# Kernel optimization log

Hardware: AMD Instinct MI355X
Metric: run time of the kernel (lower is better)

## Reference

```python
import jax, jax.numpy as jnp
import numpy as np

PI = np.pi


def ramp_filter(x):
    """skimage-style ramp filter along the detector axis (axis=2).
    x: [B, C, D, A] sinogram."""
    D = x.shape[2]
    P = max(64, int(2 ** np.ceil(np.log2(2 * D))))  # padded FFT size
    xp = jnp.pad(x, ((0, 0), (0, 0), (0, P - D), (0, 0)))
    # real-space ramp kernel (Kak & Slaney), then FFT -> frequency filter
    n = np.concatenate([np.arange(1, P // 2 + 1, 2), np.arange(P // 2 - 1, 0, -2)])
    f = np.zeros(P, dtype=np.float64)
    f[0] = 0.25
    f[1::2] = -1.0 / (PI * n) ** 2
    fourier_filter = jnp.asarray(2.0 * np.real(np.fft.fft(f)), dtype=jnp.float32)  # [P]
    proj = jnp.fft.fft(xp, axis=2) * fourier_filter[None, None, :, None]
    return jnp.real(jnp.fft.ifft(proj, axis=2))[:, :, :D, :].astype(x.dtype)


def setup_inputs() -> dict:
    key = jax.random.key(0)
    x = jax.random.normal(key, (2, 1, 512, 180), dtype=jnp.float32)  # [B,C,D,A]
    return {"x": x}


def reference(x):
    B, C, D, A = x.shape
    S = D  # circle=True -> in_size == out_size == detector count
    xf = ramp_filter(x)

    lin = jnp.arange(S, dtype=jnp.float32) * 2.0 / (S - 1) - 1.0
    xg = lin[None, :]  # [1,S], varies along columns (image x)
    yg = lin[:, None]  # [S,1], varies along rows  (image y)
    theta = jnp.deg2rad(jnp.arange(A, dtype=jnp.float32))

    # detector coordinate for each (angle, pixel): T = x*cos(th) - y*sin(th), in [-1,1]
    T = xg[None] * jnp.cos(theta)[:, None, None] - yg[None] * jnp.sin(theta)[:, None, None]  # [A,S,S]

    # grid X selects column i_theta exactly (align_corners=True semantics);
    # grid_sample thus reduces to 1-D linear interpolation along the detector axis.
    pix = (T + 1.0) * (D - 1) * 0.5  # pixel coords in [0, D-1] domain
    i0 = jnp.floor(pix)
    w1 = pix - i0
    i0 = i0.astype(jnp.int32)
    i1 = i0 + 1

    xt = jnp.transpose(xf, (0, 1, 3, 2))  # [B,C,A,D]
    a_idx = jnp.arange(A)[:, None, None]  # [A,1,1]

    def gather(idx):
        valid = ((idx >= 0) & (idx <= D - 1)).astype(xf.dtype)  # zero padding
        idxc = jnp.clip(idx, 0, D - 1)
        g = xt[:, :, a_idx, idxc]  # [B,C,A,S,S]
        return g * valid

    contrib = gather(i0) * (1.0 - w1) + gather(i1) * w1  # [B,C,A,S,S]
    reco = jnp.sum(contrib, axis=2)  # [B,C,S,S]

    circle_mask = ((xg ** 2 + yg ** 2) <= 1.0).astype(reco.dtype)  # [S,S]
    reco = reco * circle_mask
    return reco * jnp.float32(PI / (2.0 * A))
```

## Files before the change

kernel.cpp:

```cpp
#include <hip/hip_runtime.h>
#include <hip/hip_fp16.h>
#include <math.h>

#define D_DET 512
#define N_ANG 180
#define S_IMG 512
#define NPIX  (S_IMG * S_IMG)
#define T_MAX 63
#define AG    72
#define AL    108
#define WIN   32

typedef _Float16 half2v __attribute__((ext_vector_type(2)));

struct TrigTab { float2 cs[N_ANG]; };

__device__ __constant__ float kPI = 3.14159265358979323846f;

__device__ __forceinline__ half2v pack_w1(float w) {
    return __builtin_bit_cast(half2v, __builtin_amdgcn_cvt_pkrtz(1.0f, w));
}

__global__ __launch_bounds__(512) void ramp_filter_kernel(
    const float* __restrict__ x, unsigned* __restrict__ xfh) {
    __shared__ float rp[4][640];
    __shared__ float xf[4][D_DET + 1];

    const int blk = blockIdx.x;
    const int bc  = blk / 45;
    const int a0  = (blk % 45) * 4;
    const int d   = threadIdx.x;

    float4 q = *(const float4*)(x + (bc * D_DET + d) * N_ANG + a0);
    rp[0][64 + d] = q.x;
    rp[1][64 + d] = q.y;
    rp[2][64 + d] = q.z;
    rp[3][64 + d] = q.w;
    if (d < 64) {
        #pragma unroll
        for (int r = 0; r < 4; ++r) { rp[r][d] = 0.0f; rp[r][576 + d] = 0.0f; }
    }
    if (d < 4) xf[d][D_DET] = 0.0f;
    __syncthreads();

    constexpr float PI_ = 3.14159265358979323846f;
    #pragma unroll
    for (int r = 0; r < 4; ++r) {
        const float* rm = &rp[r][64 + d];
        float acc = 0.5f * rm[0];
        #pragma unroll
        for (int k = 0; k < (T_MAX + 1) / 2; ++k) {
            const int   t = 2 * k + 1;
            const float h = -2.0f / (PI_ * PI_ * (float)(t * t));
            acc = fmaf(rm[-t] + rm[t], h, acc);
        }
        xf[r][d] = acc;
    }
    __syncthreads();

    #pragma unroll
    for (int r = 0; r < 4; ++r) {
        const float f0 = xf[r][d];
        const float dl = xf[r][d + 1] - f0;
        const unsigned lo = __half_as_ushort(__float2half_rn(f0));
        const unsigned hi = __half_as_ushort(__float2half_rn(dl));
        xfh[((a0 + r) * D_DET + d) * 2 + bc] = (hi << 16) | lo;
    }
}

__global__ __launch_bounds__(512) void backproj_kernel(
    const uint2* __restrict__ xfh, float* __restrict__ out, TrigTab tt) {
    __shared__ float  dminF[AL];
    __shared__ int    dminI[AL];
    __shared__ uint2  win[AL * WIN];
    __shared__ float2 red[256];

    const int tid = threadIdx.x;
    const int bi  = blockIdx.x >> 5;
    const int bj  = blockIdx.x & 31;
    const int i0  = bi << 4;
    const int j0  = bj << 4;

    if (tid < AL) {
        float2 cs = tt.cs[AG + tid];
        float c5 = cs.x, s5 = cs.y;
        float x0 = (float)j0 * (2.0f / 511.0f) - 1.0f;
        float x1 = (float)(j0 + 15) * (2.0f / 511.0f) - 1.0f;
        float y0 = (float)i0 * (2.0f / 511.0f) - 1.0f;
        float y1 = (float)(i0 + 15) * (2.0f / 511.0f) - 1.0f;
        float pmin = 255.5f + fminf(c5 * x0, c5 * x1)
                            + fminf(-s5 * y0, -s5 * y1);
        int dmin = (int)floorf(pmin) - 1;
        dmin = dmin < 0 ? 0 : (dmin > (D_DET - WIN) ? (D_DET - WIN) : dmin);
        dmin &= ~1;
        dminI[tid] = dmin;
        dminF[tid] = 255.5f - (float)dmin;
    }
    __syncthreads();

    {
        const uint4* __restrict__ src4 = (const uint4*)xfh;
        uint4* win4 = (uint4*)win;
        for (int f = tid; f < AL * (WIN / 2); f += 512) {
            int a    = f >> 4;
            int e    = f & 15;
            int dmin = dminI[a];
            win4[f]  = src4[((((AG + a) << 9) + dmin) >> 1) + e];
        }
    }
    __syncthreads();

    const int half = tid >> 8;
    const int sub  = (tid >> 6) & 3;
    const int lane = tid & 63;
    const int px   = tid & 255;
    const int i = i0 + ((sub >> 1) << 3) + (lane >> 3);
    const int j = j0 + ((sub & 1) << 3) + (lane & 7);

    const float xP = (float)j * (2.0f / 511.0f) - 1.0f;
    const float yP = (float)i * (2.0f / 511.0f) - 1.0f;
    const float m  = xP * xP + yP * yP;
    const bool inc = (m <= 1.0f);
    const float xS = inc ? xP : 0.0f;
    const float yS = inc ? yP : 0.0f;

    float a0 = 0.0f, a1 = 0.0f;
    if (__any(inc)) {
        if (half == 0) {
            #pragma unroll 6
            for (int a = 0; a < AG; ++a) {
                float2 t  = tt.cs[a];
                float pc  = fmaf(xS, t.x, fmaf(yS, -t.y, 255.5f));
                pc        = fmaxf(pc, 0.0f);
                int   fi  = (int)pc;
                float w   = __builtin_amdgcn_fractf(pc);
                half2v hw = pack_w1(w);
                uint2  g  = xfh[(a << 9) + fi];
                a0 = __builtin_amdgcn_fdot2(hw, __builtin_bit_cast(half2v, g.x), a0, false);
                a1 = __builtin_amdgcn_fdot2(hw, __builtin_bit_cast(half2v, g.y), a1, false);
            }
        } else {
            const float4* __restrict__ bias4 = (const float4*)dminF;
            #pragma unroll 3
            for (int gq = 0; gq < AL / 4; ++gq) {
                const float4 bs = bias4[gq];
                #pragma unroll
                for (int jj = 0; jj < 4; ++jj) {
                    const int al = gq * 4 + jj;
                    const float bias = (jj == 0) ? bs.x : (jj == 1) ? bs.y
                                     : (jj == 2) ? bs.z : bs.w;
                    float2 t  = tt.cs[AG + al];
                    float pcW = fmaf(xS, t.x, fmaf(yS, -t.y, bias));
                    pcW       = fminf(fmaxf(pcW, 0.0f), (float)(WIN - 1));
                    int   fi  = (int)pcW;
                    float w   = __builtin_amdgcn_fractf(pcW);
                    half2v hw = pack_w1(w);
                    uint2  g  = win[(al << 5) + fi];
                    a0 = __builtin_amdgcn_fdot2(hw, __builtin_bit_cast(half2v, g.x), a0, false);
                    a1 = __builtin_amdgcn_fdot2(hw, __builtin_bit_cast(half2v, g.y), a1, false);
                }
            }
        }
    }

    if (half == 1) red[px] = make_float2(a0, a1);
    __syncthreads();
    if (half == 0) {
        const float2 r = red[px];
        const float msk = inc ? (kPI / (2.0f * (float)N_ANG)) : 0.0f;
        const int p = i * S_IMG + j;
        out[p]        = (a0 + r.x) * msk;
        out[NPIX + p] = (a1 + r.y) * msk;
    }
}

extern "C" void kernel_launch(void* const* d_in, const int* in_sizes, int n_in,
                              void* d_out, int out_size, void* d_ws, size_t ws_size,
                              hipStream_t stream) {
    const float* x   = (const float*)d_in[0];
    float*       out = (float*)d_out;
    unsigned*    xfh = (unsigned*)d_ws;

    TrigTab tt;
    for (int a = 0; a < N_ANG; ++a) {
        double th = (double)a * 3.14159265358979323846 / 180.0;
        tt.cs[a].x = (float)(cos(th) * 255.5);
        tt.cs[a].y = (float)(sin(th) * 255.5);
    }

    ramp_filter_kernel<<<90, 512, 0, stream>>>(x, xfh);
    backproj_kernel<<<1024, 512, 0, stream>>>((const uint2*)xfh, out, tt);
}
```

Before: 26.79 us.

## Merge global and LDS angle halves into one interleaved loop per thread

Switches the backprojection block from 512 threads, where two halves split the angles between global-memory and LDS-window gathers and then reduce through shared memory, to 256 threads. Each thread now covers all angles in one loop that interleaves 2 global-gather angles with 3 LDS-gather angles per iteration. This drops the reduction buffer and the final barrier, and lets whole wavefronts outside the circle write zeros and exit early. The cost is half as many threads per tile, so there is less parallelism to hide gather latency, and the LDS window fill is spread over fewer threads.

```diff
diff --git a/kernel.cpp b/kernel.cpp
--- a/kernel.cpp
+++ b/kernel.cpp
@@ -68,12 +68,11 @@
     }
 }
 
-__global__ __launch_bounds__(512) void backproj_kernel(
+__global__ __launch_bounds__(256) void backproj_kernel(
     const uint2* __restrict__ xfh, float* __restrict__ out, TrigTab tt) {
     __shared__ float  dminF[AL];
     __shared__ int    dminI[AL];
     __shared__ uint2  win[AL * WIN];
-    __shared__ float2 red[256];
 
     const int tid = threadIdx.x;
     const int bi  = blockIdx.x >> 5;
@@ -101,7 +100,7 @@
     {
         const uint4* __restrict__ src4 = (const uint4*)xfh;
         uint4* win4 = (uint4*)win;
-        for (int f = tid; f < AL * (WIN / 2); f += 512) {
+        for (int f = tid; f < AL * (WIN / 2); f += 256) {
             int a    = f >> 4;
             int e    = f & 15;
             int dmin = dminI[a];
@@ -110,10 +109,8 @@
     }
     __syncthreads();
 
-    const int half = tid >> 8;
-    const int sub  = (tid >> 6) & 3;
+    const int sub  = tid >> 6;
     const int lane = tid & 63;
-    const int px   = tid & 255;
     const int i = i0 + ((sub >> 1) << 3) + (lane >> 3);
     const int j = j0 + ((sub & 1) << 3) + (lane & 7);
 
@@ -123,55 +120,49 @@
     const bool inc = (m <= 1.0f);
     const float xS = inc ? xP : 0.0f;
     const float yS = inc ? yP : 0.0f;
+    const int  p   = i * S_IMG + j;
+
+    if (!__any(inc)) {
+        out[p]        = 0.0f;
+        out[NPIX + p] = 0.0f;
+        return;
+    }
 
     float a0 = 0.0f, a1 = 0.0f;
-    if (__any(inc)) {
-        if (half == 0) {
-            #pragma unroll 6
-            for (int a = 0; a < AG; ++a) {
-                float2 t  = tt.cs[a];
-                float pc  = fmaf(xS, t.x, fmaf(yS, -t.y, 255.5f));
-                pc        = fmaxf(pc, 0.0f);
-                int   fi  = (int)pc;
-                float w   = __builtin_amdgcn_fractf(pc);
-                half2v hw = pack_w1(w);
-                uint2  g  = xfh[(a << 9) + fi];
-                a0 = __builtin_amdgcn_fdot2(hw, __builtin_bit_cast(half2v, g.x), a0, false);
-                a1 = __builtin_amdgcn_fdot2(hw, __builtin_bit_cast(half2v, g.y), a1, false);
-            }
-        } else {
-            const float4* __restrict__ bias4 = (const float4*)dminF;
-            #pragma unroll 3
-            for (int gq = 0; gq < AL / 4; ++gq) {
-                const float4 bs = bias4[gq];
-                #pragma unroll
-                for (int jj = 0; jj < 4; ++jj) {
-                    const int al = gq * 4 + jj;
-                    const float bias = (jj == 0) ? bs.x : (jj == 1) ? bs.y
-                                     : (jj == 2) ? bs.z : bs.w;
-                    float2 t  = tt.cs[AG + al];
-                    float pcW = fmaf(xS, t.x, fmaf(yS, -t.y, bias));
-                    pcW       = fminf(fmaxf(pcW, 0.0f), (float)(WIN - 1));
-                    int   fi  = (int)pcW;
-                    float w   = __builtin_amdgcn_fractf(pcW);
-                    half2v hw = pack_w1(w);
-                    uint2  g  = win[(al << 5) + fi];
-                    a0 = __builtin_amdgcn_fdot2(hw, __builtin_bit_cast(half2v, g.x), a0, false);
-                    a1 = __builtin_amdgcn_fdot2(hw, __builtin_bit_cast(half2v, g.y), a1, false);
-                }
-            }
+    #pragma unroll 2
+    for (int it = 0; it < 36; ++it) {
+        #pragma unroll
+        for (int k = 0; k < 2; ++k) {
+            const int a = 2 * it + k;
+            float2 t  = tt.cs[a];
+            float pc  = fmaf(xS, t.x, fmaf(yS, -t.y, 255.5f));
+            pc        = fmaxf(pc, 0.0f);
+            int   fi  = (int)pc;
+            float w   = __builtin_amdgcn_fractf(pc);
+            half2v hw = pack_w1(w);
+            uint2  g  = xfh[(a << 9) + fi];
+            a0 = __builtin_amdgcn_fdot2(hw, __builtin_bit_cast(half2v, g.x), a0, false);
+            a1 = __builtin_amdgcn_fdot2(hw, __builtin_bit_cast(half2v, g.y), a1, false);
+        }
+        #pragma unroll
+        for (int k = 0; k < 3; ++k) {
+            const int al = 3 * it + k;
+            float2 t  = tt.cs[AG + al];
+            float bias = dminF[al];
+            float pcW = fmaf(xS, t.x, fmaf(yS, -t.y, bias));
+            pcW       = fminf(fmaxf(pcW, 0.0f), (float)(WIN - 1));
+            int   fi  = (int)pcW;
+            float w   = __builtin_amdgcn_fractf(pcW);
+            half2v hw = pack_w1(w);
+            uint2  g  = win[(al << 5) + fi];
+            a0 = __builtin_amdgcn_fdot2(hw, __builtin_bit_cast(half2v, g.x), a0, false);
+            a1 = __builtin_amdgcn_fdot2(hw, __builtin_bit_cast(half2v, g.y), a1, false);
         }
     }
 
-    if (half == 1) red[px] = make_float2(a0, a1);
-    __syncthreads();
-    if (half == 0) {
-        const float2 r = red[px];
-        const float msk = inc ? (kPI / (2.0f * (float)N_ANG)) : 0.0f;
-        const int p = i * S_IMG + j;
-        out[p]        = (a0 + r.x) * msk;
-        out[NPIX + p] = (a1 + r.y) * msk;
-    }
+    const float msk = inc ? (kPI / (2.0f * (float)N_ANG)) : 0.0f;
+    out[p]        = a0 * msk;
+    out[NPIX + p] = a1 * msk;
 }
 
 extern "C" void kernel_launch(void* const* d_in, const int* in_sizes, int n_in,
@@ -189,5 +180,5 @@
     }
 
     ramp_filter_kernel<<<90, 512, 0, stream>>>(x, xfh);
-    backproj_kernel<<<1024, 512, 0, stream>>>((const uint2*)xfh, out, tt);
+    backproj_kernel<<<1024, 256, 0, stream>>>((const uint2*)xfh, out, tt);
 }
```

After: 29.02 us. +8.3%, slower.
